# Kernel tuning notes

Measured on AMD Instinct MI355X. Metric: run time of the kernel, lower is better.

Reference implementation:

```python
import jax, jax.numpy as jnp
import numpy as np

N = 100000      # nodes
E = 1600000     # edges (avg degree 16)
IN = 128
OUT = 256


def setup_inputs() -> dict:
    key = jax.random.key(0)
    ks = jax.random.split(key, 8)
    x = jax.random.normal(ks[0], (N, IN), dtype=jnp.float32)
    edge_index = jax.random.randint(ks[1], (2, E), 0, N, dtype=jnp.int64)
    # GCNConv weights (glorot-ish scale) and biases
    W1 = jax.random.normal(ks[2], (IN, OUT), dtype=jnp.float32) / np.float32(np.sqrt(IN))
    b1 = jnp.zeros((OUT,), jnp.float32)
    W2 = jax.random.normal(ks[3], (OUT, OUT), dtype=jnp.float32) / np.float32(np.sqrt(OUT))
    b2 = jnp.zeros((OUT,), jnp.float32)
    # projection Linear(IN, OUT)
    Wp = jax.random.normal(ks[4], (IN, OUT), dtype=jnp.float32) / np.float32(np.sqrt(IN))
    bp = jax.random.normal(ks[5], (OUT,), dtype=jnp.float32) * 0.01
    return {"x": x, "edge_index": edge_index, "W1": W1, "b1": b1,
            "W2": W2, "b2": b2, "Wp": Wp, "bp": bp}


def _gcn_conv(x, W, b, src, dst, n):
    """PyG GCNConv: D^{-1/2}(A+I)D^{-1/2} X W + b. src/dst already include self-loops."""
    xw = x @ W                                              # [n, out]
    ones = jnp.ones(src.shape[0], dtype=xw.dtype)
    deg = jax.ops.segment_sum(ones, dst, num_segments=n)    # in-degree incl. self-loop
    dinv = jnp.where(deg > 0, jax.lax.rsqrt(deg), 0.0)
    norm = dinv[src] * dinv[dst]                            # [e]
    msgs = xw[src] * norm[:, None]                          # gather + scale
    out = jax.ops.segment_sum(msgs, dst, num_segments=n)    # scatter-add
    return out + b


def reference(x, edge_index, W1, b1, W2, b2, Wp, bp):
    n = x.shape[0]
    loop = jnp.arange(n, dtype=edge_index.dtype)            # self-loops
    src = jnp.concatenate([edge_index[0], loop])
    dst = jnp.concatenate([edge_index[1], loop])
    out = jax.nn.relu(_gcn_conv(x, W1, b1, src, dst, n))
    out = _gcn_conv(out, W2, b2, src, dst, n)
    identity = x @ Wp + bp                                  # projection (IN != OUT)
    return jax.nn.relu(out + identity)
```

## Files before the change

### kernel.cpp

```cpp
#include <hip/hip_runtime.h>

#define NODES 100000
#define EDGES 1600000
#define FIN   128
#define FOUT  256
#define NBUCK 196

typedef __bf16 bf16;
typedef __bf16 bf16x8 __attribute__((ext_vector_type(8)));
typedef __bf16 bf16x4 __attribute__((ext_vector_type(4)));
typedef __bf16 bf16x2 __attribute__((ext_vector_type(2)));
typedef float  f32x4  __attribute__((ext_vector_type(4)));

__global__ __launch_bounds__(256) void detect_kernel(const void* __restrict__ x,
                                                     const int* __restrict__ ei,
                                                     int* __restrict__ flags) {
    __shared__ int s_f32_evidence;
    __shared__ int s_odd_nonzero;
    int t = threadIdx.x;
    if (t == 0) { s_f32_evidence = 0; s_odd_nonzero = 0; }
    __syncthreads();
    const bf16* xb = (const bf16*)x;
    int local_f32 = 0;
    for (int i = t; i < 4096; i += 256) {
        float v = fabsf((float)xb[i]);
        if (!(v < 1e4f)) local_f32 = 1;
    }
    if (local_f32) atomicOr(&s_f32_evidence, 1);
    int local_odd = 0;
    for (int k = t; k < 1024; k += 256) {
        if (ei[2 * k + 1] != 0) local_odd = 1;
    }
    if (local_odd) atomicOr(&s_odd_nonzero, 1);
    __syncthreads();
    if (t == 0) {
        flags[0] = s_f32_evidence ? 0 : 1;
        flags[1] = s_odd_nonzero ? 0 : 1;
    }
}

__device__ __forceinline__ int edge_at(const int* __restrict__ ei, int which, int i,
                                       int is64) {
    if (is64) return ei[2 * (which * EDGES + i)];
    return ei[which * EDGES + i];
}

__global__ __launch_bounds__(512) void deg_count(const int* __restrict__ ei,
                                                 int* __restrict__ deg,
                                                 int* __restrict__ bhist,
                                                 const int* __restrict__ flags) {
    __shared__ int lh[256];
    int t = threadIdx.x;
    if (t < 256) lh[t] = 0;
    __syncthreads();
    int i = blockIdx.x * 512 + t;
    if (i < EDGES) {
        int is64 = flags[1];
        int s = edge_at(ei, 0, i, is64);
        int d = edge_at(ei, 1, i, is64);
        if (s >= 0 && s < NODES && d >= 0 && d < NODES) {
            atomicAdd(&deg[d], 1);
            atomicAdd(&lh[d >> 9], 1);
        }
    }
    __syncthreads();
    if (t < NBUCK && lh[t] > 0) atomicAdd(&bhist[t], lh[t]);
}

__global__ __launch_bounds__(256) void deg_to_dinv(const int* __restrict__ deg,
                                                   float* __restrict__ dinv, int n) {
    int i = blockIdx.x * 256 + threadIdx.x;
    if (i < n) dinv[i] = rsqrtf((float)deg[i] + 1.0f);
}

__global__ __launch_bounds__(1024) void scan1(const int* __restrict__ deg,
                                              int* __restrict__ col_ptr,
                                              int* __restrict__ blksum, int n) {
    __shared__ int sm[1024];
    int t = threadIdx.x;
    int i = blockIdx.x * 1024 + t;
    int v = (i < n) ? deg[i] : 0;
    sm[t] = v;
    __syncthreads();
    for (int off = 1; off < 1024; off <<= 1) {
        int u = (t >= off) ? sm[t - off] : 0;
        __syncthreads();
        sm[t] += u;
        __syncthreads();
    }
    if (i <= n) col_ptr[i] = sm[t] - v;
    if (t == 1023) blksum[blockIdx.x] = sm[t];
}

__global__ __launch_bounds__(128) void scan2(int* blk, int nblk) {
    __shared__ int sm[128];
    int t = threadIdx.x;
    int v = (t < nblk) ? blk[t] : 0;
    sm[t] = v;
    __syncthreads();
    for (int off = 1; off < 128; off <<= 1) {
        int u = (t >= off) ? sm[t - off] : 0;
        __syncthreads();
        sm[t] += u;
        __syncthreads();
    }
    if (t < nblk) blk[t] = sm[t] - v;
}

__global__ __launch_bounds__(256) void scan3(int* __restrict__ col_ptr,
                                             const int* __restrict__ blkoff, int n) {
    int i = blockIdx.x * 256 + threadIdx.x;
    if (i <= n) col_ptr[i] += blkoff[i >> 10];
}

__global__ __launch_bounds__(256) void bucket_scan(const int* __restrict__ bhist,
                                                   int* __restrict__ bbase,
                                                   int* __restrict__ bcur) {
    __shared__ int sm[256];
    int t = threadIdx.x;
    int v = (t < NBUCK) ? bhist[t] : 0;
    sm[t] = v;
    __syncthreads();
    for (int off = 1; off < 256; off <<= 1) {
        int u = (t >= off) ? sm[t - off] : 0;
        __syncthreads();
        sm[t] += u;
        __syncthreads();
    }
    if (t < NBUCK) {
        int ex = sm[t] - v;
        bbase[t] = ex;
        bcur[t]  = ex;
        if (t == NBUCK - 1) bbase[NBUCK] = sm[t];
    }
}

#define EPB 4096
__global__ __launch_bounds__(256) void partition_edges(const int* __restrict__ ei,
                                                       int* __restrict__ bcur,
                                                       uint2* __restrict__ pairs,
                                                       const int* __restrict__ flags) {
    __shared__ int lh[256], sc[256], lst[256], lcu[256], gb[256];
    __shared__ uint2 stage[EPB];
    int t = threadIdx.x;
    int base = blockIdx.x * EPB;
    int is64 = flags[1];

    lh[t] = 0;
    __syncthreads();

    int es[16], ed[16];
#pragma unroll
    for (int j = 0; j < 16; ++j) {
        int i = base + j * 256 + t;
        int s = -1, d = -1;
        if (i < EDGES) {
            s = edge_at(ei, 0, i, is64);
            d = edge_at(ei, 1, i, is64);
            if (s < 0 || s >= NODES || d < 0 || d >= NODES) d = -1;
        }
        es[j] = s; ed[j] = d;
        if (d >= 0) atomicAdd(&lh[d >> 9], 1);
    }
    __syncthreads();
    sc[t] = lh[t];
    __syncthreads();
    for (int off = 1; off < 256; off <<= 1) {
        int u = (t >= off) ? sc[t - off] : 0;
        __syncthreads();
        sc[t] += u;
        __syncthreads();
    }
    int start = sc[t] - lh[t];
    lst[t] = start;
    lcu[t] = start;
    __syncthreads();
#pragma unroll
    for (int j = 0; j < 16; ++j) {
        if (ed[j] >= 0) {
            int p = atomicAdd(&lcu[ed[j] >> 9], 1);
            stage[p] = make_uint2((unsigned)es[j], (unsigned)ed[j]);
        }
    }
    __syncthreads();
    if (t < NBUCK && lh[t] > 0) gb[t] = atomicAdd(&bcur[t], lh[t]);
    __syncthreads();
    int nval = sc[255];
    for (int slot = t; slot < nval; slot += 256) {
        uint2 e = stage[slot];
        int b = (int)(e.y >> 9);
        pairs[(size_t)gb[b] + (slot - lst[b])] = e;
    }
}

__global__ __launch_bounds__(512) void fine_fill(const uint2* __restrict__ pairs,
                                                 const int* __restrict__ bbase,
                                                 const int* __restrict__ col_ptr,
                                                 int* __restrict__ col_idx) {
    __shared__ int lcur[512];
    int b = blockIdx.x;
    int t = threadIdx.x;
    int node = (b << 9) + t;
    lcur[t] = (node < NODES) ? col_ptr[node] : 0;
    __syncthreads();
    int beg = bbase[b], end = bbase[b + 1];
    for (int i = beg + t; i < end; i += 512) {
        uint2 e = pairs[i];
        int pos = atomicAdd(&lcur[e.y & 511], 1);
        col_idx[pos] = (int)e.x;
    }
}

__global__ __launch_bounds__(256) void pack_all(const void* __restrict__ W1,
                                                const void* __restrict__ W2,
                                                const void* __restrict__ Wp,
                                                const void* __restrict__ b1,
                                                const void* __restrict__ b2,
                                                const void* __restrict__ bp,
                                                bf16* __restrict__ W1p, bf16* __restrict__ W2p,
                                                bf16* __restrict__ Wpp, bf16* __restrict__ b1b,
                                                bf16* __restrict__ b2b, bf16* __restrict__ bpb,
                                                const int* __restrict__ flags) {
    int fl = flags[0];
    int b = blockIdx.x;
    if (b < 512) {
        const void* W; bf16* Wo; int idx;
        if (b < 128)      { W = W1; Wo = W1p; idx = b * 256 + threadIdx.x; }
        else if (b < 384) { W = W2; Wo = W2p; idx = (b - 128) * 256 + threadIdx.x; }
        else              { W = Wp; Wo = Wpp; idx = (b - 384) * 256 + threadIdx.x; }
        int j    = idx & 7;
        int lane = (idx >> 3) & 63;
        int ct   = (idx >> 9) & 15;
        int kt   = idx >> 13;
        int k = kt * 32 + (lane >> 4) * 8 + j;
        int n = ct * 16 + (lane & 15);
        Wo[idx] = fl ? ((const bf16*)W)[k * 256 + n]
                     : (bf16)(((const float*)W)[k * 256 + n]);
    } else {
        const void* bb; bf16* bo;
        if (b == 512)      { bb = b1; bo = b1b; }
        else if (b == 513) { bb = b2; bo = b2b; }
        else               { bb = bp; bo = bpb; }
        int i = threadIdx.x;
        bo[i] = fl ? ((const bf16*)bb)[i] : (bf16)(((const float*)bb)[i]);
    }
}

__global__ __launch_bounds__(256) void gemm_proj(const void* __restrict__ Av,
                                                 const bf16* __restrict__ Wpk,
                                                 const float* __restrict__ dinv,
                                                 const bf16* __restrict__ bias,
                                                 void* __restrict__ outv,
                                                 bf16* __restrict__ Xs,
                                                 const int* __restrict__ flags) {
    int a_f32 = (flags[0] == 0);
    int wave = threadIdx.x >> 6;
    int lane = threadIdx.x & 63;
    int row0 = blockIdx.x * 64;
    int lr = lane & 15;
    int lk = (lane >> 4) * 8;

    int arow[4];
    float di4[4];
#pragma unroll
    for (int rf = 0; rf < 4; ++rf) {
        int r = row0 + rf * 16 + lr;
        arow[rf] = r < NODES ? r : (NODES - 1);
        di4[rf] = dinv[arow[rf]];
    }

    f32x4 acc[4][4];
    f32x4 z = {0.f, 0.f, 0.f, 0.f};
#pragma unroll
    for (int i = 0; i < 4; ++i)
#pragma unroll
        for (int j = 0; j < 4; ++j) acc[i][j] = z;

    for (int kt = 0; kt < 4; ++kt) {
        bf16x8 af[4];
        if (!a_f32) {
            const bf16* Ab = (const bf16*)Av + kt * 32 + lk;
#pragma unroll
            for (int rf = 0; rf < 4; ++rf)
                af[rf] = *(const bf16x8*)(Ab + (size_t)arow[rf] * FIN);
        } else {
            const float* Af = (const float*)Av + kt * 32 + lk;
#pragma unroll
            for (int rf = 0; rf < 4; ++rf) {
                const float* p = Af + (size_t)arow[rf] * FIN;
                f32x4 lo = *(const f32x4*)p;
                f32x4 hi = *(const f32x4*)(p + 4);
                af[rf][0] = (bf16)lo[0]; af[rf][1] = (bf16)lo[1];
                af[rf][2] = (bf16)lo[2]; af[rf][3] = (bf16)lo[3];
                af[rf][4] = (bf16)hi[0]; af[rf][5] = (bf16)hi[1];
                af[rf][6] = (bf16)hi[2]; af[rf][7] = (bf16)hi[3];
            }
        }
#pragma unroll
        for (int rf = 0; rf < 4; ++rf) {
            bf16x8 xsv;
#pragma unroll
            for (int j = 0; j < 8; ++j) xsv[j] = (bf16)(di4[rf] * (float)af[rf][j]);
            *(bf16x8*)(Xs + (size_t)arow[rf] * FIN + kt * 32 + lk) = xsv;
        }
        const bf16* wb = Wpk + ((size_t)(kt * 16 + wave * 4) * 64 + lane) * 8;
        bf16x8 bfv[4];
#pragma unroll
        for (int cf = 0; cf < 4; ++cf)
            bfv[cf] = *(const bf16x8*)(wb + cf * 512);
#pragma unroll
        for (int rf = 0; rf < 4; ++rf)
#pragma unroll
            for (int cf = 0; cf < 4; ++cf)
                acc[rf][cf] = __builtin_amdgcn_mfma_f32_16x16x32_bf16(
                    af[rf], bfv[cf], acc[rf][cf], 0, 0, 0);
    }

    int rb = (lane >> 4) * 4;
    int out_f32 = a_f32;
#pragma unroll
    for (int rf = 0; rf < 4; ++rf) {
#pragma unroll
        for (int r = 0; r < 4; ++r) {
            int row = row0 + rf * 16 + rb + r;
            if (row >= NODES) continue;
#pragma unroll
            for (int cf = 0; cf < 4; ++cf) {
                int col = wave * 64 + cf * 16 + lr;
                float v = acc[rf][cf][r] + (float)bias[col];
                size_t off = (size_t)row * 256 + col;
                if (out_f32) ((float*)outv)[off] = v;
                else         ((bf16*)outv)[off]  = (bf16)v;
            }
        }
    }
}

__global__ __launch_bounds__(256) void gemm_tile(const bf16* __restrict__ A,
                                                 const bf16* __restrict__ Wpk,
                                                 int K,
                                                 const float* __restrict__ dinv,
                                                 const bf16* __restrict__ bias,
                                                 int relu,
                                                 bf16* __restrict__ out) {
    int wave = threadIdx.x >> 6;
    int lane = threadIdx.x & 63;
    int row0 = blockIdx.x * 64;
    int lr = lane & 15;
    int lk = (lane >> 4) * 8;

    int arow[4];
#pragma unroll
    for (int rf = 0; rf < 4; ++rf) {
        int r = row0 + rf * 16 + lr;
        arow[rf] = r < NODES ? r : (NODES - 1);
    }

    f32x4 acc[4][4];
    f32x4 z = {0.f, 0.f, 0.f, 0.f};
#pragma unroll
    for (int i = 0; i < 4; ++i)
#pragma unroll
        for (int j = 0; j < 4; ++j) acc[i][j] = z;

    int ktiles = K >> 5;
    for (int kt = 0; kt < ktiles; ++kt) {
        const bf16* Ab = A + kt * 32 + lk;
        bf16x8 af[4];
#pragma unroll
        for (int rf = 0; rf < 4; ++rf)
            af[rf] = *(const bf16x8*)(Ab + (size_t)arow[rf] * K);
        const bf16* wb = Wpk + ((size_t)(kt * 16 + wave * 4) * 64 + lane) * 8;
        bf16x8 bfv[4];
#pragma unroll
        for (int cf = 0; cf < 4; ++cf)
            bfv[cf] = *(const bf16x8*)(wb + cf * 512);
#pragma unroll
        for (int rf = 0; rf < 4; ++rf)
#pragma unroll
            for (int cf = 0; cf < 4; ++cf)
                acc[rf][cf] = __builtin_amdgcn_mfma_f32_16x16x32_bf16(
                    af[rf], bfv[cf], acc[rf][cf], 0, 0, 0);
    }

    int rb = (lane >> 4) * 4;
#pragma unroll
    for (int rf = 0; rf < 4; ++rf) {
#pragma unroll
        for (int r = 0; r < 4; ++r) {
            int row = row0 + rf * 16 + rb + r;
            if (row >= NODES) continue;
            float s = dinv ? dinv[row] : 1.0f;
#pragma unroll
            for (int cf = 0; cf < 4; ++cf) {
                int col = wave * 64 + cf * 16 + lr;
                float v = acc[rf][cf][r] * s;
                if (bias) v += (float)bias[col];
                if (relu) v = fmaxf(v, 0.0f);
                out[(size_t)row * 256 + col] = (bf16)v;
            }
        }
    }
}

__global__ __launch_bounds__(256) void gather1(const int* __restrict__ col_ptr,
                                               const int* __restrict__ col_idx,
                                               const bf16* __restrict__ Xs,
                                               const float* __restrict__ dinv,
                                               bf16* __restrict__ aggX) {
    int wid  = (int)((blockIdx.x * 256 + threadIdx.x) >> 6);
    int lane = threadIdx.x & 63;
    if (wid >= NODES) return;
    int beg = col_ptr[wid], end = col_ptr[wid + 1];
    int c2 = lane * 2;

    float a0 = 0.f, a1 = 0.f;
    for (int chunk = beg; chunk < end; chunk += 64) {
        int cnt = end - chunk;
        if (cnt > 64) cnt = 64;
        int myidx = (lane < cnt) ? col_idx[chunk + lane] : 0;
        int j = 0;
        for (; j + 8 <= cnt; j += 8) {
            bf16x2 v[8];
#pragma unroll
            for (int u = 0; u < 8; ++u) {
                int s = __shfl(myidx, j + u);
                v[u] = *(const bf16x2*)(Xs + (size_t)s * FIN + c2);
            }
#pragma unroll
            for (int u = 0; u < 8; ++u) { a0 += (float)v[u][0]; a1 += (float)v[u][1]; }
        }
        for (; j < cnt; ++j) {
            int s = __shfl(myidx, j);
            bf16x2 v = *(const bf16x2*)(Xs + (size_t)s * FIN + c2);
            a0 += (float)v[0]; a1 += (float)v[1];
        }
    }

    bf16x2 self = *(const bf16x2*)(Xs + (size_t)wid * FIN + c2);
    float di = dinv[wid];
    bf16x2 o;
    o[0] = (bf16)(di * (a0 + (float)self[0]));
    o[1] = (bf16)(di * (a1 + (float)self[1]));
    *(bf16x2*)(aggX + (size_t)wid * FIN + c2) = o;
}

__global__ __launch_bounds__(256) void gather2(const int* __restrict__ col_ptr,
                                               const int* __restrict__ col_idx,
                                               const bf16* __restrict__ Y2,
                                               const float* __restrict__ dinv,
                                               const bf16* __restrict__ bias,
                                               const void* __restrict__ proj,
                                               void* __restrict__ outv,
                                               const int* __restrict__ flags) {
    int io_f32 = (flags[0] == 0);
    int wid  = (int)((blockIdx.x * 256 + threadIdx.x) >> 6);
    int lane = threadIdx.x & 63;
    if (wid >= NODES) return;
    int beg = col_ptr[wid], end = col_ptr[wid + 1];
    int c = lane * 4;

    f32x4 acc = {0.f, 0.f, 0.f, 0.f};
    for (int chunk = beg; chunk < end; chunk += 64) {
        int cnt = end - chunk;
        if (cnt > 64) cnt = 64;
        int myidx = (lane < cnt) ? col_idx[chunk + lane] : 0;
        int j = 0;
        for (; j + 8 <= cnt; j += 8) {
            bf16x4 v[8];
#pragma unroll
            for (int u = 0; u < 8; ++u) {
                int s = __shfl(myidx, j + u);
                v[u] = *(const bf16x4*)(Y2 + (size_t)s * 256 + c);
            }
#pragma unroll
            for (int u = 0; u < 8; ++u)
#pragma unroll
                for (int k = 0; k < 4; ++k) acc[k] += (float)v[u][k];
        }
        for (; j < cnt; ++j) {
            int s = __shfl(myidx, j);
            bf16x4 v = *(const bf16x4*)(Y2 + (size_t)s * 256 + c);
#pragma unroll
            for (int k = 0; k < 4; ++k) acc[k] += (float)v[k];
        }
    }

    bf16x4 selfv = *(const bf16x4*)(Y2 + (size_t)wid * 256 + c);
    float di = dinv[wid];
    size_t base = (size_t)wid * 256 + c;

    f32x4 res;
#pragma unroll
    for (int k = 0; k < 4; ++k)
        res[k] = di * (acc[k] + (float)selfv[k]) + (float)bias[c + k];

    if (io_f32) {
        f32x4 pv = *(const f32x4*)((const float*)proj + base);
        f32x4 o;
#pragma unroll
        for (int k = 0; k < 4; ++k) o[k] = fmaxf(res[k] + pv[k], 0.0f);
        *(f32x4*)((float*)outv + base) = o;
    } else {
        bf16x4 pv = *(const bf16x4*)((const bf16*)proj + base);
        bf16x4 o;
#pragma unroll
        for (int k = 0; k < 4; ++k) o[k] = (bf16)fmaxf(res[k] + (float)pv[k], 0.0f);
        *(bf16x4*)((bf16*)outv + base) = o;
    }
}

__global__ __launch_bounds__(256) void zero_out(bf16* out, int nelem) {
    int i = blockIdx.x * 256 + threadIdx.x;
    if (i < nelem) out[i] = (bf16)0.0f;
}

extern "C" void kernel_launch(void* const* d_in, const int* in_sizes, int n_in,
                              void* d_out, int out_size, void* d_ws, size_t ws_size,
                              hipStream_t stream) {
    const void* x   = d_in[0];
    const int*  ei  = (const int*)d_in[1];
    const void* W1  = d_in[2];
    const void* b1  = d_in[3];
    const void* W2  = d_in[4];
    const void* b2  = d_in[5];
    const void* Wp  = d_in[6];
    const void* bp  = d_in[7];

    const size_t NEEDED = 401408ull * 3 + 1024ull * 4 + 6400000 + 65536 + 131072 + 65536
                        + 1536 + 25600000ull * 2 + 51200000ull;
    if (ws_size < NEEDED) {
        zero_out<<<(NODES * 256 + 255) / 256, 256, 0, stream>>>((bf16*)d_out, NODES * 256);
        return;
    }
    char* w = (char*)d_ws;
    int*   col_ptr = (int*)w;   w += 401408;
    int*   deg     = (int*)w;   w += 401408;
    int*   bhist   = (int*)w;   w += 1024;
    float* dinv    = (float*)w; w += 401408;
    int*   blk     = (int*)w;   w += 1024;
    int*   flags   = (int*)w;   w += 1024;
    int*   bbase   = (int*)w;   w += 1024;
    int*   bcur    = (int*)w;   w += 1024;
    int*   col_idx = (int*)w;   w += 6400000;
    bf16*  W1p     = (bf16*)w;  w += 65536;
    bf16*  W2p     = (bf16*)w;  w += 131072;
    bf16*  Wpp     = (bf16*)w;  w += 65536;
    bf16*  b1b     = (bf16*)w;  w += 512;
    bf16*  b2b     = (bf16*)w;  w += 512;
    bf16*  bpb     = (bf16*)w;  w += 512;
    bf16*  Xs      = (bf16*)w;  w += 25600000;
    bf16*  aggX    = (bf16*)w;  w += 25600000;
    bf16*  H1      = (bf16*)w;  w += 51200000;
    uint2* pairs   = (uint2*)Xs;
    bf16*  Y2      = Xs;

    const int NBLK = (NODES + 1 + 1023) / 1024;

    detect_kernel<<<1, 256, 0, stream>>>(x, ei, flags);

    hipMemsetAsync(deg, 0, 401408 + 1024, stream);
    deg_count<<<(EDGES + 511) / 512, 512, 0, stream>>>(ei, deg, bhist, flags);
    deg_to_dinv<<<(NODES + 255) / 256, 256, 0, stream>>>(deg, dinv, NODES);

    scan1<<<NBLK, 1024, 0, stream>>>(deg, col_ptr, blk, NODES);
    scan2<<<1, 128, 0, stream>>>(blk, NBLK);
    scan3<<<(NODES + 256) / 256, 256, 0, stream>>>(col_ptr, blk, NODES);
    bucket_scan<<<1, 256, 0, stream>>>(bhist, bbase, bcur);

    partition_edges<<<(EDGES + EPB - 1) / EPB, 256, 0, stream>>>(ei, bcur, pairs, flags);
    fine_fill<<<NBUCK, 512, 0, stream>>>(pairs, bbase, col_ptr, col_idx);

    pack_all<<<515, 256, 0, stream>>>(W1, W2, Wp, b1, b2, bp,
                                      W1p, W2p, Wpp, b1b, b2b, bpb, flags);

    const int gemm_grid   = (NODES + 63) / 64;
    const int gather_grid = (NODES + 3) / 4;

    gemm_proj<<<gemm_grid, 256, 0, stream>>>(x, Wpp, dinv, bpb, d_out, Xs, flags);
    gather1<<<gather_grid, 256, 0, stream>>>(col_ptr, col_idx, Xs, dinv, aggX);
    gemm_tile<<<gemm_grid, 256, 0, stream>>>(aggX, W1p, FIN, nullptr, b1b, 1, H1);
    gemm_tile<<<gemm_grid, 256, 0, stream>>>(H1, W2p, FOUT, dinv, nullptr, 0, Y2);
    gather2<<<gather_grid, 256, 0, stream>>>(col_ptr, col_idx, Y2, dinv, b2b,
                                             d_out, d_out, flags);
}
```

Baseline: 667.0 us.

## Widen gather loads to 16-byte vectors, fuse small scan kernels, add nontemporal stores

```diff
diff --git a/kernel.cpp b/kernel.cpp
--- a/kernel.cpp
+++ b/kernel.cpp
@@ -9,7 +9,6 @@
 typedef __bf16 bf16;
 typedef __bf16 bf16x8 __attribute__((ext_vector_type(8)));
 typedef __bf16 bf16x4 __attribute__((ext_vector_type(4)));
-typedef __bf16 bf16x2 __attribute__((ext_vector_type(2)));
 typedef float  f32x4  __attribute__((ext_vector_type(4)));
 
 __global__ __launch_bounds__(256) void detect_kernel(const void* __restrict__ x,
@@ -67,19 +66,15 @@
     if (t < NBUCK && lh[t] > 0) atomicAdd(&bhist[t], lh[t]);
 }
 
-__global__ __launch_bounds__(256) void deg_to_dinv(const int* __restrict__ deg,
-                                                   float* __restrict__ dinv, int n) {
-    int i = blockIdx.x * 256 + threadIdx.x;
-    if (i < n) dinv[i] = rsqrtf((float)deg[i] + 1.0f);
-}
-
 __global__ __launch_bounds__(1024) void scan1(const int* __restrict__ deg,
                                               int* __restrict__ col_ptr,
-                                              int* __restrict__ blksum, int n) {
+                                              int* __restrict__ blksum,
+                                              float* __restrict__ dinv, int n) {
     __shared__ int sm[1024];
     int t = threadIdx.x;
     int i = blockIdx.x * 1024 + t;
     int v = (i < n) ? deg[i] : 0;
+    if (i < n) dinv[i] = rsqrtf((float)v + 1.0f);
     sm[t] = v;
     __syncthreads();
     for (int off = 1; off < 1024; off <<= 1) {
@@ -92,47 +87,46 @@
     if (t == 1023) blksum[blockIdx.x] = sm[t];
 }
 
-__global__ __launch_bounds__(128) void scan2(int* blk, int nblk) {
-    __shared__ int sm[128];
+__global__ __launch_bounds__(256) void scan_small(int* __restrict__ blk, int nblk,
+                                                  const int* __restrict__ bhist,
+                                                  int* __restrict__ bbase,
+                                                  int* __restrict__ bcur) {
+    __shared__ int sm[256];
     int t = threadIdx.x;
-    int v = (t < nblk) ? blk[t] : 0;
-    sm[t] = v;
-    __syncthreads();
-    for (int off = 1; off < 128; off <<= 1) {
-        int u = (t >= off) ? sm[t - off] : 0;
+    if (blockIdx.x == 0) {
+        int v = (t < nblk) ? blk[t] : 0;
+        sm[t] = v;
         __syncthreads();
-        sm[t] += u;
+        for (int off = 1; off < 256; off <<= 1) {
+            int u = (t >= off) ? sm[t - off] : 0;
+            __syncthreads();
+            sm[t] += u;
+            __syncthreads();
+        }
+        if (t < nblk) blk[t] = sm[t] - v;
+    } else {
+        int v = (t < NBUCK) ? bhist[t] : 0;
+        sm[t] = v;
         __syncthreads();
-    }
-    if (t < nblk) blk[t] = sm[t] - v;
+        for (int off = 1; off < 256; off <<= 1) {
+            int u = (t >= off) ? sm[t - off] : 0;
+            __syncthreads();
+            sm[t] += u;
+            __syncthreads();
+        }
+        if (t < NBUCK) {
+            int ex = sm[t] - v;
+            bbase[t] = ex;
+            bcur[t]  = ex;
+            if (t == NBUCK - 1) bbase[NBUCK] = sm[t];
+        }
+    }
 }
 
 __global__ __launch_bounds__(256) void scan3(int* __restrict__ col_ptr,
                                              const int* __restrict__ blkoff, int n) {
     int i = blockIdx.x * 256 + threadIdx.x;
     if (i <= n) col_ptr[i] += blkoff[i >> 10];
-}
-
-__global__ __launch_bounds__(256) void bucket_scan(const int* __restrict__ bhist,
-                                                   int* __restrict__ bbase,
-                                                   int* __restrict__ bcur) {
-    __shared__ int sm[256];
-    int t = threadIdx.x;
-    int v = (t < NBUCK) ? bhist[t] : 0;
-    sm[t] = v;
-    __syncthreads();
-    for (int off = 1; off < 256; off <<= 1) {
-        int u = (t >= off) ? sm[t - off] : 0;
-        __syncthreads();
-        sm[t] += u;
-        __syncthreads();
-    }
-    if (t < NBUCK) {
-        int ex = sm[t] - v;
-        bbase[t] = ex;
-        bcur[t]  = ex;
-        if (t == NBUCK - 1) bbase[NBUCK] = sm[t];
-    }
 }
 
 #define EPB 4096
@@ -329,7 +323,7 @@
                 int col = wave * 64 + cf * 16 + lr;
                 float v = acc[rf][cf][r] + (float)bias[col];
                 size_t off = (size_t)row * 256 + col;
-                if (out_f32) ((float*)outv)[off] = v;
+                if (out_f32) __builtin_nontemporal_store(v, (float*)outv + off);
                 else         ((bf16*)outv)[off]  = (bf16)v;
             }
         }
@@ -411,38 +405,51 @@
     int wid  = (int)((blockIdx.x * 256 + threadIdx.x) >> 6);
     int lane = threadIdx.x & 63;
     if (wid >= NODES) return;
+    int q  = lane >> 4;
+    int li = lane & 15;
+    int c8 = li * 8;
     int beg = col_ptr[wid], end = col_ptr[wid + 1];
-    int c2 = lane * 2;
-
-    float a0 = 0.f, a1 = 0.f;
+
+    float acc[8] = {0.f, 0.f, 0.f, 0.f, 0.f, 0.f, 0.f, 0.f};
     for (int chunk = beg; chunk < end; chunk += 64) {
         int cnt = end - chunk;
         if (cnt > 64) cnt = 64;
         int myidx = (lane < cnt) ? col_idx[chunk + lane] : 0;
         int j = 0;
-        for (; j + 8 <= cnt; j += 8) {
-            bf16x2 v[8];
-#pragma unroll
-            for (int u = 0; u < 8; ++u) {
-                int s = __shfl(myidx, j + u);
-                v[u] = *(const bf16x2*)(Xs + (size_t)s * FIN + c2);
-            }
-#pragma unroll
-            for (int u = 0; u < 8; ++u) { a0 += (float)v[u][0]; a1 += (float)v[u][1]; }
-        }
-        for (; j < cnt; ++j) {
-            int s = __shfl(myidx, j);
-            bf16x2 v = *(const bf16x2*)(Xs + (size_t)s * FIN + c2);
-            a0 += (float)v[0]; a1 += (float)v[1];
-        }
-    }
-
-    bf16x2 self = *(const bf16x2*)(Xs + (size_t)wid * FIN + c2);
-    float di = dinv[wid];
-    bf16x2 o;
-    o[0] = (bf16)(di * (a0 + (float)self[0]));
-    o[1] = (bf16)(di * (a1 + (float)self[1]));
-    *(bf16x2*)(aggX + (size_t)wid * FIN + c2) = o;
+        for (; j + 16 <= cnt; j += 16) {
+            bf16x8 v[4];
+#pragma unroll
+            for (int l = 0; l < 4; ++l) {
+                int s = __shfl(myidx, j + 4 * l + q);
+                v[l] = *(const bf16x8*)(Xs + (size_t)s * FIN + c8);
+            }
+#pragma unroll
+            for (int l = 0; l < 4; ++l)
+#pragma unroll
+                for (int k = 0; k < 8; ++k) acc[k] += (float)v[l][k];
+        }
+        for (; j < cnt; j += 4) {
+            if (j + q < cnt) {
+                int s = __shfl(myidx, j + q);
+                bf16x8 v = *(const bf16x8*)(Xs + (size_t)s * FIN + c8);
+#pragma unroll
+                for (int k = 0; k < 8; ++k) acc[k] += (float)v[k];
+            }
+        }
+    }
+#pragma unroll
+    for (int k = 0; k < 8; ++k) {
+        acc[k] += __shfl_xor(acc[k], 16);
+        acc[k] += __shfl_xor(acc[k], 32);
+    }
+    if (q == 0) {
+        bf16x8 self = *(const bf16x8*)(Xs + (size_t)wid * FIN + c8);
+        float di = dinv[wid];
+        bf16x8 o;
+#pragma unroll
+        for (int k = 0; k < 8; ++k) o[k] = (bf16)(di * (acc[k] + (float)self[k]));
+        *(bf16x8*)(aggX + (size_t)wid * FIN + c8) = o;
+    }
 }
 
 __global__ __launch_bounds__(256) void gather2(const int* __restrict__ col_ptr,
@@ -457,56 +464,70 @@
     int wid  = (int)((blockIdx.x * 256 + threadIdx.x) >> 6);
     int lane = threadIdx.x & 63;
     if (wid >= NODES) return;
+    int half = lane >> 5;
+    int li   = lane & 31;
+    int c8   = li * 8;
     int beg = col_ptr[wid], end = col_ptr[wid + 1];
-    int c = lane * 4;
-
-    f32x4 acc = {0.f, 0.f, 0.f, 0.f};
+
+    float acc[8] = {0.f, 0.f, 0.f, 0.f, 0.f, 0.f, 0.f, 0.f};
     for (int chunk = beg; chunk < end; chunk += 64) {
         int cnt = end - chunk;
         if (cnt > 64) cnt = 64;
         int myidx = (lane < cnt) ? col_idx[chunk + lane] : 0;
         int j = 0;
-        for (; j + 8 <= cnt; j += 8) {
-            bf16x4 v[8];
-#pragma unroll
-            for (int u = 0; u < 8; ++u) {
-                int s = __shfl(myidx, j + u);
-                v[u] = *(const bf16x4*)(Y2 + (size_t)s * 256 + c);
-            }
-#pragma unroll
-            for (int u = 0; u < 8; ++u)
-#pragma unroll
-                for (int k = 0; k < 4; ++k) acc[k] += (float)v[u][k];
-        }
-        for (; j < cnt; ++j) {
-            int s = __shfl(myidx, j);
-            bf16x4 v = *(const bf16x4*)(Y2 + (size_t)s * 256 + c);
-#pragma unroll
-            for (int k = 0; k < 4; ++k) acc[k] += (float)v[k];
-        }
-    }
-
-    bf16x4 selfv = *(const bf16x4*)(Y2 + (size_t)wid * 256 + c);
-    float di = dinv[wid];
-    size_t base = (size_t)wid * 256 + c;
-
-    f32x4 res;
-#pragma unroll
-    for (int k = 0; k < 4; ++k)
-        res[k] = di * (acc[k] + (float)selfv[k]) + (float)bias[c + k];
-
-    if (io_f32) {
-        f32x4 pv = *(const f32x4*)((const float*)proj + base);
-        f32x4 o;
-#pragma unroll
-        for (int k = 0; k < 4; ++k) o[k] = fmaxf(res[k] + pv[k], 0.0f);
-        *(f32x4*)((float*)outv + base) = o;
-    } else {
-        bf16x4 pv = *(const bf16x4*)((const bf16*)proj + base);
-        bf16x4 o;
-#pragma unroll
-        for (int k = 0; k < 4; ++k) o[k] = (bf16)fmaxf(res[k] + (float)pv[k], 0.0f);
-        *(bf16x4*)((bf16*)outv + base) = o;
+        for (; j + 16 <= cnt; j += 16) {
+            bf16x8 v[8];
+#pragma unroll
+            for (int l = 0; l < 8; ++l) {
+                int s = __shfl(myidx, j + 2 * l + half);
+                v[l] = *(const bf16x8*)(Y2 + (size_t)s * 256 + c8);
+            }
+#pragma unroll
+            for (int l = 0; l < 8; ++l)
+#pragma unroll
+                for (int k = 0; k < 8; ++k) acc[k] += (float)v[l][k];
+        }
+        for (; j < cnt; j += 2) {
+            if (j + half < cnt) {
+                int s = __shfl(myidx, j + half);
+                bf16x8 v = *(const bf16x8*)(Y2 + (size_t)s * 256 + c8);
+#pragma unroll
+                for (int k = 0; k < 8; ++k) acc[k] += (float)v[k];
+            }
+        }
+    }
+#pragma unroll
+    for (int k = 0; k < 8; ++k) acc[k] += __shfl_xor(acc[k], 32);
+
+    if (half == 0) {
+        bf16x8 selfv = *(const bf16x8*)(Y2 + (size_t)wid * 256 + c8);
+        float di = dinv[wid];
+        size_t base = (size_t)wid * 256 + c8;
+        float res[8];
+#pragma unroll
+        for (int k = 0; k < 8; ++k)
+            res[k] = di * (acc[k] + (float)selfv[k]) + (float)bias[c8 + k];
+        if (io_f32) {
+            const float* pp = (const float*)proj + base;
+            f32x4 p0 = __builtin_nontemporal_load((const f32x4*)pp);
+            f32x4 p1 = __builtin_nontemporal_load((const f32x4*)(pp + 4));
+            f32x4 o0, o1;
+#pragma unroll
+            for (int k = 0; k < 4; ++k) {
+                o0[k] = fmaxf(res[k] + p0[k], 0.0f);
+                o1[k] = fmaxf(res[k + 4] + p1[k], 0.0f);
+            }
+            float* op = (float*)outv + base;
+            __builtin_nontemporal_store(o0, (f32x4*)op);
+            __builtin_nontemporal_store(o1, (f32x4*)(op + 4));
+        } else {
+            bf16x8 pv = *(const bf16x8*)((const bf16*)proj + base);
+            bf16x8 o;
+#pragma unroll
+            for (int k = 0; k < 8; ++k)
+                o[k] = (bf16)fmaxf(res[k] + (float)pv[k], 0.0f);
+            *(bf16x8*)((bf16*)outv + base) = o;
+        }
     }
 }
 
@@ -561,12 +582,10 @@
 
     hipMemsetAsync(deg, 0, 401408 + 1024, stream);
     deg_count<<<(EDGES + 511) / 512, 512, 0, stream>>>(ei, deg, bhist, flags);
-    deg_to_dinv<<<(NODES + 255) / 256, 256, 0, stream>>>(deg, dinv, NODES);
-
-    scan1<<<NBLK, 1024, 0, stream>>>(deg, col_ptr, blk, NODES);
-    scan2<<<1, 128, 0, stream>>>(blk, NBLK);
+
+    scan1<<<NBLK, 1024, 0, stream>>>(deg, col_ptr, blk, dinv, NODES);
+    scan_small<<<2, 256, 0, stream>>>(blk, NBLK, bhist, bbase, bcur);
     scan3<<<(NODES + 256) / 256, 256, 0, stream>>>(col_ptr, blk, NODES);
-    bucket_scan<<<1, 256, 0, stream>>>(bhist, bbase, bcur);
 
     partition_edges<<<(EDGES + EPB - 1) / EPB, 256, 0, stream>>>(ei, bcur, pairs, flags);
     fine_fill<<<NBUCK, 512, 0, stream>>>(pairs, bbase, col_ptr, col_idx);
```

New measurement: 674.6 us. No clear change (+1.1%).
